# Kernel tuning notes

Hardware: AMD Instinct MI355X
Metric: run time of the kernel (lower is better)

## Reference

```python
import jax, jax.numpy as jnp
import numpy as np

HEAD_SIZE = 16  # matches init_kwargs head_size


def _rope_angles(seq_len, half_dim, base=10000.0):
    # standard RoPE frequencies, matches typical precompute_pos_cis
    freqs = 1.0 / (base ** (np.arange(0, half_dim, dtype=np.float32) / half_dim))
    t = np.arange(seq_len, dtype=np.float32)
    ang = np.outer(t, freqs)  # (S, half_dim)
    return jnp.asarray(np.cos(ang)), jnp.asarray(np.sin(ang))


def setup_inputs() -> dict:
    key = jax.random.key(0)
    ks = jax.random.split(key, 10)
    B, S, D = 2, 2048, 1024
    hd = D // HEAD_SIZE
    pos_cos, pos_sin = _rope_angles(S, hd // 2)
    w = lambda k: jax.random.normal(k, (D, D), jnp.float32) * 0.02
    b = lambda k: jax.random.normal(k, (D,), jnp.float32) * 0.02
    return {
        "x": jax.random.normal(ks[0], (B, S, D), jnp.float32),
        "pos_cos": pos_cos,
        "pos_sin": pos_sin,
        "wq_w": w(ks[1]), "wq_b": b(ks[2]),
        "wk_w": w(ks[3]), "wk_b": b(ks[4]),
        "wv_w": w(ks[5]), "wv_b": b(ks[6]),
        "wo_w": w(ks[7]), "wo_b": b(ks[8]),
    }


def _apply_rope(t, cos, sin):
    # t: (B, S, H, hd); cos/sin: (S, hd//2) -> broadcast (1, S, 1, hd//2)
    B, S, H, hd = t.shape
    tr = t.reshape(B, S, H, hd // 2, 2)
    a, b = tr[..., 0], tr[..., 1]
    c = cos[None, :, None, :]
    s = sin[None, :, None, :]
    # complex multiply (a + ib) * (c + is)
    out_r = a * c - b * s
    out_i = a * s + b * c
    return jnp.stack([out_r, out_i], axis=-1).reshape(B, S, H, hd)


def reference(x, pos_cos, pos_sin, wq_w, wq_b, wk_w, wk_b, wv_w, wv_b, wo_w, wo_b):
    B, S, D = x.shape
    H = HEAD_SIZE
    hd = D // H
    q = (x @ wq_w.T + wq_b).reshape(B, S, H, hd)
    k = (x @ wk_w.T + wk_b).reshape(B, S, H, hd)
    v = (x @ wv_w.T + wv_b).reshape(B, S, H, hd)
    q = _apply_rope(q, pos_cos, pos_sin)
    k = _apply_rope(k, pos_cos, pos_sin)
    scale = 1.0 / jnp.sqrt(jnp.asarray(hd, x.dtype))
    scores = jnp.einsum('bshd,bthd->bhst', q, k) * scale  # (B,H,S,S)
    causal = jnp.tril(jnp.ones((S, S), bool))
    scores = jnp.where(causal[None, None], scores, jnp.asarray(-jnp.inf, scores.dtype))
    probs = jax.nn.softmax(scores, axis=-1)
    out = jnp.einsum('bhst,bthd->bshd', probs, v).reshape(B, S, D)
    return out @ wo_w.T + wo_b
```

## Files before the change

kernel.cpp:

```cpp
#include <hip/hip_runtime.h>
#include <stdint.h>
#include <stddef.h>


typedef __bf16 bf16x8 __attribute__((ext_vector_type(8)));
typedef float  f32x4  __attribute__((ext_vector_type(4)));

__device__ __forceinline__ unsigned short f2b(float f) {
  union { float f; uint32_t u; } v; v.f = f;
  uint32_t u = v.u;
  return (unsigned short)((u + 0x7FFFu + ((u >> 16) & 1u)) >> 16);
}

__device__ __forceinline__ void async16(const void* g, void* l) {
  __builtin_amdgcn_global_load_lds(
      (const __attribute__((address_space(1))) void*)g,
      (__attribute__((address_space(3))) void*)l, 16, 0, 0);
}

__global__ void cast_kernel(const float* __restrict__ in,
                            unsigned short* __restrict__ out, int n4) {
  int i = blockIdx.x * blockDim.x + threadIdx.x;
  if (i >= n4) return;
  float4 v = ((const float4*)in)[i];
  ushort4 o;
  o.x = f2b(v.x); o.y = f2b(v.y); o.z = f2b(v.z); o.w = f2b(v.w);
  ((ushort4*)out)[i] = o;
}

__global__ void cast_w_kernel(const float* __restrict__ wq, const float* __restrict__ wk,
                              const float* __restrict__ wv, const float* __restrict__ wo,
                              unsigned short* __restrict__ wqkv,
                              unsigned short* __restrict__ wobf) {
  int i = blockIdx.x * blockDim.x + threadIdx.x;
  const int sel = i >> 18, k = i & ((1 << 18) - 1);
  const float* src = (sel == 0) ? wq : (sel == 1) ? wk : (sel == 2) ? wv : wo;
  float4 v = ((const float4*)src)[k];
  ushort4 o;
  o.x = f2b(v.x); o.y = f2b(v.y); o.z = f2b(v.z); o.w = f2b(v.w);
  if (sel < 3) ((ushort4*)wqkv)[(size_t)sel * 262144 + k] = o;
  else         ((ushort4*)wobf)[k] = o;
}

__global__ __launch_bounds__(256) void qkv_gemm_kernel(
    const unsigned short* __restrict__ A,
    const unsigned short* __restrict__ W,
    const float* __restrict__ biasq, const float* __restrict__ biask,
    const float* __restrict__ biasv,
    const float* __restrict__ cp, const float* __restrict__ sp,
    unsigned short* __restrict__ qo,
    unsigned short* __restrict__ ko,
    unsigned short* __restrict__ vo)
{
  __shared__ unsigned short As[128 * 64];
  __shared__ unsigned short Bs[128 * 64];
  const int tid  = threadIdx.x;
  const int w    = tid >> 6, l = tid & 63;
  const int lm   = l & 15,  quad = l >> 4;
  const int nblk = blockIdx.x;
  const int m0   = blockIdx.y * 128;
  const int n0g  = nblk * 128;
  const int wm   = (w >> 1) * 64, wn = (w & 1) * 64;

  const f32x4 fzero = {0.f, 0.f, 0.f, 0.f};
  f32x4 acc[4][4];
#pragma unroll
  for (int i = 0; i < 4; ++i)
#pragma unroll
    for (int j = 0; j < 4; ++j) acc[i][j] = fzero;

  for (int k0 = 0; k0 < 1024; k0 += 64) {
    __syncthreads();
#pragma unroll
    for (int q = 0; q < 4; ++q) {
      const int row = w * 16 + lm + (q & 1) * 64;
      const int kc  = quad + (q >> 1) * 4;
      const size_t ldsb = ((size_t)(w + 4 * (q & 1)) * 128 + 64 * (q >> 1)) * 8;
      async16(A + (size_t)(m0 + row) * 1024 + k0 + kc * 8, As + ldsb);
      async16(W + (size_t)(n0g + row) * 1024 + k0 + kc * 8, Bs + ldsb);
    }
    __syncthreads();
#pragma unroll
    for (int kk = 0; kk < 2; ++kk) {
      bf16x8 af[4], bfc[4];
#pragma unroll
      for (int i = 0; i < 4; ++i)
        af[i] = *(const bf16x8*)(As + (size_t)((((w >> 1) * 4 + i) * 128 + kk * 64 + l)) * 8);
#pragma unroll
      for (int j = 0; j < 4; ++j)
        bfc[j] = *(const bf16x8*)(Bs + (size_t)((((w & 1) * 4 + j) * 128 + kk * 64 + l)) * 8);
#pragma unroll
      for (int i = 0; i < 4; ++i)
#pragma unroll
        for (int j = 0; j < 4; ++j)
          acc[i][j] = __builtin_amdgcn_mfma_f32_16x16x32_bf16(af[i], bfc[j], acc[i][j], 0, 0, 0);
    }
  }

  const int which = nblk >> 3;
  const int n0    = (nblk & 7) * 128;
  const float* bias = (which == 0) ? biasq : (which == 1) ? biask : biasv;
#pragma unroll
  for (int i = 0; i < 4; ++i) {
#pragma unroll
    for (int j = 0; j < 4; ++j) {
      const int n = n0 + wn + j * 16 + lm;
      const float bval = bias[n];
      const int h = n >> 6, d = n & 63;
      float vals[4];
#pragma unroll
      for (int r = 0; r < 4; ++r) {
        const int m = m0 + wm + i * 16 + quad * 4 + r;
        const int srow = m & 2047;
        float val = acc[i][j][r] + bval;
        if (which != 2) {
          const float c  = cp[srow * 32 + (d >> 1)];
          const float sn = sp[srow * 32 + (d >> 1)];
          const float part = __shfl_xor(val, 1, 64);
          val = (d & 1) ? (part * sn + val * c) : (val * c - part * sn);
        }
        vals[r] = val;
      }
      const int mbase = m0 + wm + i * 16 + quad * 4;
      const int b = mbase >> 11, s0 = mbase & 2047;
      const int bh = (b << 4) + h;
      if (which == 0) {
#pragma unroll
        for (int r = 0; r < 4; ++r)
          qo[((size_t)bh * 2048 + s0 + r) * 64 + d] = f2b(vals[r]);
      } else if (which == 1) {
#pragma unroll
        for (int r = 0; r < 4; ++r) {
          const int s = s0 + r;
          ko[((size_t)bh * 32 + (s >> 6)) * 4096 +
             (size_t)(((d >> 3) * 64 + (s & 63))) * 8 + (d & 7)] = f2b(vals[r]);
        }
      } else {
        uint32_t w0 = (uint32_t)f2b(vals[0]) | ((uint32_t)f2b(vals[1]) << 16);
        uint32_t w1 = (uint32_t)f2b(vals[2]) | ((uint32_t)f2b(vals[3]) << 16);
        uint2 pk; pk.x = w0; pk.y = w1;
        *(uint2*)(vo + ((size_t)bh * 32 + (s0 >> 6)) * 4096 +
                  (size_t)((((s0 & 63) >> 3) * 64 + d)) * 8 + (s0 & 7)) = pk;
      }
    }
  }
}

__global__ __launch_bounds__(512, 4) void flash_kernel(
    const unsigned short* __restrict__ Q,
    const unsigned short* __restrict__ K,
    const unsigned short* __restrict__ VT,
    unsigned short* __restrict__ O)
{
  constexpr int PSTRIDE = 72;
  __shared__ unsigned short Ks[4096];
  __shared__ unsigned short Vs[4096];
  __shared__ unsigned short Ps[128 * PSTRIDE];
  const int tid = threadIdx.x;
  const int w = tid >> 6, l = tid & 63, lm = l & 15, quad = l >> 4;
  const int bh = blockIdx.x, qb = 15 - blockIdx.y;
  const int mrow_g = qb * 128 + w * 16 + lm;

  const size_t qbase = ((size_t)bh * 2048 + (size_t)qb * 128) * 64;
  bf16x8 aq[2];
#pragma unroll
  for (int kc = 0; kc < 2; ++kc)
    aq[kc] = *(const bf16x8*)(Q + qbase + (size_t)(w * 16 + lm) * 64 + kc * 32 + quad * 8);

  const f32x4 fzero = {0.f, 0.f, 0.f, 0.f};
  f32x4 Oacc[4];
#pragma unroll
  for (int jo = 0; jo < 4; ++jo) Oacc[jo] = fzero;
  float m_i = -1e30f, l_i = 0.f;

  const int nkv = 2 * qb + 2;
  for (int kt = 0; kt < nkv; ++kt) {
    __syncthreads();
    {
      const size_t tbase = ((size_t)bh * 32 + kt) * 4096;
      async16(K  + tbase + (size_t)tid * 8, Ks + (size_t)w * 512);
      async16(VT + tbase + (size_t)tid * 8, Vs + (size_t)w * 512);
    }
    __syncthreads();

    f32x4 Sc[4];
#pragma unroll
    for (int tb = 0; tb < 4; ++tb) Sc[tb] = fzero;
#pragma unroll
    for (int kc = 0; kc < 2; ++kc) {
      bf16x8 ak[4];
#pragma unroll
      for (int tb = 0; tb < 4; ++tb)
        ak[tb] = *(const bf16x8*)(Ks + (size_t)(((kc * 4 + quad) * 64 + tb * 16 + lm)) * 8);
#pragma unroll
      for (int tb = 0; tb < 4; ++tb)
        Sc[tb] = __builtin_amdgcn_mfma_f32_16x16x32_bf16(ak[tb], aq[kc], Sc[tb], 0, 0, 0);
    }

    const bool needmask = (kt * 64 + 63 > qb * 128 + w * 16);
    const int  mrel = mrow_g - kt * 64;
    float mx = -1e30f;
#pragma unroll
    for (int tb = 0; tb < 4; ++tb) {
#pragma unroll
      for (int r = 0; r < 4; ++r) {
        float s = Sc[tb][r] * 0.125f;
        if (needmask && (tb * 16 + quad * 4 + r > mrel)) s = -1e30f;
        Sc[tb][r] = s;
        mx = fmaxf(mx, s);
      }
    }
    mx = fmaxf(mx, __shfl_xor(mx, 16, 64));
    mx = fmaxf(mx, __shfl_xor(mx, 32, 64));
    const float mnew  = fmaxf(m_i, mx);
    const float alpha = __expf(m_i - mnew);
    m_i = mnew;

    float ps = 0.f;
#pragma unroll
    for (int tb = 0; tb < 4; ++tb) {
      float p0 = __expf(Sc[tb][0] - mnew), p1 = __expf(Sc[tb][1] - mnew);
      float p2 = __expf(Sc[tb][2] - mnew), p3 = __expf(Sc[tb][3] - mnew);
      ps += (p0 + p1) + (p2 + p3);
      uint2 pk;
      pk.x = (uint32_t)f2b(p0) | ((uint32_t)f2b(p1) << 16);
      pk.y = (uint32_t)f2b(p2) | ((uint32_t)f2b(p3) << 16);
      *(uint2*)(Ps + (size_t)(w * 16 + lm) * PSTRIDE + tb * 16 + quad * 4) = pk;
    }
    ps += __shfl_xor(ps, 16, 64);
    ps += __shfl_xor(ps, 32, 64);
    l_i = l_i * alpha + ps;

    float af4[4];
#pragma unroll
    for (int r = 0; r < 4; ++r) af4[r] = __shfl(alpha, quad * 4 + r, 64);
#pragma unroll
    for (int jo = 0; jo < 4; ++jo)
#pragma unroll
      for (int r = 0; r < 4; ++r) Oacc[jo][r] *= af4[r];

#pragma unroll
    for (int kc = 0; kc < 2; ++kc) {
      bf16x8 ap = *(const bf16x8*)(Ps + (size_t)(w * 16 + lm) * PSTRIDE + kc * 32 + quad * 8);
      bf16x8 bv[4];
#pragma unroll
      for (int jo = 0; jo < 4; ++jo)
        bv[jo] = *(const bf16x8*)(Vs + (size_t)(((kc * 4 + quad) * 64 + jo * 16 + lm)) * 8);
#pragma unroll
      for (int jo = 0; jo < 4; ++jo)
        Oacc[jo] = __builtin_amdgcn_mfma_f32_16x16x32_bf16(ap, bv[jo], Oacc[jo], 0, 0, 0);
    }
  }

  float lf[4];
#pragma unroll
  for (int r = 0; r < 4; ++r) lf[r] = 1.0f / __shfl(l_i, quad * 4 + r, 64);
  const int b = bh >> 4, h = bh & 15;
#pragma unroll
  for (int jo = 0; jo < 4; ++jo)
#pragma unroll
    for (int r = 0; r < 4; ++r) {
      const int s   = qb * 128 + w * 16 + quad * 4 + r;
      const int col = h * 64 + jo * 16 + lm;
      O[((size_t)b * 2048 + s) * 1024 + col] = f2b(Oacc[jo][r] * lf[r]);
    }
}

__global__ __launch_bounds__(256) void oproj_gemm_kernel(
    const unsigned short* __restrict__ A,
    const unsigned short* __restrict__ W,
    const float* __restrict__ bias,
    float* __restrict__ out)
{
  __shared__ unsigned short As[64 * 64];
  __shared__ unsigned short Bs[128 * 64];
  const int tid = threadIdx.x;
  const int w = tid >> 6, l = tid & 63;
  const int lm = l & 15, quad = l >> 4;
  const int m0 = blockIdx.y * 64;
  const int n0 = blockIdx.x * 128;

  const f32x4 fzero = {0.f, 0.f, 0.f, 0.f};
  f32x4 acc[4][2];
#pragma unroll
  for (int i = 0; i < 4; ++i)
#pragma unroll
    for (int j = 0; j < 2; ++j) acc[i][j] = fzero;

  for (int k0 = 0; k0 < 1024; k0 += 64) {
    __syncthreads();
#pragma unroll
    for (int q = 0; q < 2; ++q) {
      const int row = w * 16 + lm;
      const int kc  = quad + 4 * q;
      async16(A + (size_t)(m0 + row) * 1024 + k0 + kc * 8,
              As + ((size_t)w * 128 + 64 * q) * 8);
    }
#pragma unroll
    for (int q = 0; q < 4; ++q) {
      const int row = w * 16 + lm + (q & 1) * 64;
      const int kc  = quad + 4 * (q >> 1);
      async16(W + (size_t)(n0 + row) * 1024 + k0 + kc * 8,
              Bs + ((size_t)(w + 4 * (q & 1)) * 128 + 64 * (q >> 1)) * 8);
    }
    __syncthreads();
#pragma unroll
    for (int kk = 0; kk < 2; ++kk) {
      bf16x8 af[4], bfc[2];
#pragma unroll
      for (int i = 0; i < 4; ++i)
        af[i] = *(const bf16x8*)(As + (size_t)((i * 128 + kk * 64 + l)) * 8);
#pragma unroll
      for (int j = 0; j < 2; ++j)
        bfc[j] = *(const bf16x8*)(Bs + (size_t)(((w * 2 + j) * 128 + kk * 64 + l)) * 8);
#pragma unroll
      for (int i = 0; i < 4; ++i)
#pragma unroll
        for (int j = 0; j < 2; ++j)
          acc[i][j] = __builtin_amdgcn_mfma_f32_16x16x32_bf16(af[i], bfc[j], acc[i][j], 0, 0, 0);
    }
  }

#pragma unroll
  for (int i = 0; i < 4; ++i) {
#pragma unroll
    for (int j = 0; j < 2; ++j) {
      const int n = n0 + w * 32 + j * 16 + lm;
      const float bval = bias[n];
#pragma unroll
      for (int r = 0; r < 4; ++r) {
        const int m = m0 + i * 16 + quad * 4 + r;
        out[(size_t)m * 1024 + n] = acc[i][j][r] + bval;
      }
    }
  }
}

extern "C" void kernel_launch(void* const* d_in, const int* in_sizes, int n_in,
                              void* d_out, int out_size, void* d_ws, size_t ws_size,
                              hipStream_t stream) {
  (void)in_sizes; (void)n_in; (void)out_size; (void)ws_size;
  const float* x  = (const float*)d_in[0];
  const float* cp = (const float*)d_in[1];
  const float* sp = (const float*)d_in[2];
  const float* wq = (const float*)d_in[3];
  const float* bq = (const float*)d_in[4];
  const float* wk = (const float*)d_in[5];
  const float* bk = (const float*)d_in[6];
  const float* wv = (const float*)d_in[7];
  const float* bv = (const float*)d_in[8];
  const float* wo = (const float*)d_in[9];
  const float* bo = (const float*)d_in[10];
  float* out = (float*)d_out;

  unsigned short* xbf  = (unsigned short*)d_ws;
  unsigned short* wqkv = xbf  + (size_t)4 * 1024 * 1024;
  unsigned short* wobf = wqkv + (size_t)3 * 1024 * 1024;
  unsigned short* qbf  = wobf + (size_t)1 * 1024 * 1024;
  unsigned short* kbf  = qbf  + (size_t)4 * 1024 * 1024;
  unsigned short* vbf  = kbf  + (size_t)4 * 1024 * 1024;
  unsigned short* obf  = vbf  + (size_t)4 * 1024 * 1024;

  hipLaunchKernelGGL(cast_kernel, dim3(4096), dim3(256), 0, stream, x, xbf, 1048576);
  hipLaunchKernelGGL(cast_w_kernel, dim3(4096), dim3(256), 0, stream,
                     wq, wk, wv, wo, wqkv, wobf);

  hipLaunchKernelGGL(qkv_gemm_kernel, dim3(24, 32), dim3(256), 0, stream,
                     xbf, wqkv, bq, bk, bv, cp, sp, qbf, kbf, vbf);
  hipLaunchKernelGGL(flash_kernel, dim3(32, 16), dim3(512), 0, stream,
                     qbf, kbf, vbf, obf);
  hipLaunchKernelGGL(oproj_gemm_kernel, dim3(8, 64), dim3(256), 0, stream,
                     obf, wobf, bo, out);
}
```

Baseline: 240.1 us.

## Double-buffer LDS tiles in QKV GEMM, flash attention, and output projection

Doubles the shared-memory tiles in the QKV GEMM, flash attention, and output-projection kernels. The next K-slice or KV tile is issued asynchronously before computing on the current one, and one barrier per iteration replaces two. This is meant to hide global-to-LDS load latency behind MFMA work. It doubles the LDS footprint per block, which can reduce occupancy, and compiler-inserted waits on async loads may limit the overlap.

```diff
diff --git a/kernel.cpp b/kernel.cpp
--- a/kernel.cpp
+++ b/kernel.cpp
@@ -52,8 +52,8 @@
     unsigned short* __restrict__ ko,
     unsigned short* __restrict__ vo)
 {
-  __shared__ unsigned short As[128 * 64];
-  __shared__ unsigned short Bs[128 * 64];
+  __shared__ unsigned short As[2][128 * 64];
+  __shared__ unsigned short Bs[2][128 * 64];
   const int tid  = threadIdx.x;
   const int w    = tid >> 6, l = tid & 63;
   const int lm   = l & 15,  quad = l >> 4;
@@ -69,33 +69,44 @@
 #pragma unroll
     for (int j = 0; j < 4; ++j) acc[i][j] = fzero;
 
-  for (int k0 = 0; k0 < 1024; k0 += 64) {
-    __syncthreads();
+  auto stage_tile = [&](int buf, int k0) {
 #pragma unroll
     for (int q = 0; q < 4; ++q) {
       const int row = w * 16 + lm + (q & 1) * 64;
       const int kc  = quad + (q >> 1) * 4;
       const size_t ldsb = ((size_t)(w + 4 * (q & 1)) * 128 + 64 * (q >> 1)) * 8;
-      async16(A + (size_t)(m0 + row) * 1024 + k0 + kc * 8, As + ldsb);
-      async16(W + (size_t)(n0g + row) * 1024 + k0 + kc * 8, Bs + ldsb);
-    }
-    __syncthreads();
+      async16(A + (size_t)(m0 + row) * 1024 + k0 + kc * 8, &As[buf][ldsb]);
+      async16(W + (size_t)(n0g + row) * 1024 + k0 + kc * 8, &Bs[buf][ldsb]);
+    }
+  };
+  auto compute_tile = [&](int buf) {
 #pragma unroll
     for (int kk = 0; kk < 2; ++kk) {
       bf16x8 af[4], bfc[4];
 #pragma unroll
       for (int i = 0; i < 4; ++i)
-        af[i] = *(const bf16x8*)(As + (size_t)((((w >> 1) * 4 + i) * 128 + kk * 64 + l)) * 8);
+        af[i] = *(const bf16x8*)(&As[buf][(size_t)((((w >> 1) * 4 + i) * 128 + kk * 64 + l)) * 8]);
 #pragma unroll
       for (int j = 0; j < 4; ++j)
-        bfc[j] = *(const bf16x8*)(Bs + (size_t)((((w & 1) * 4 + j) * 128 + kk * 64 + l)) * 8);
+        bfc[j] = *(const bf16x8*)(&Bs[buf][(size_t)((((w & 1) * 4 + j) * 128 + kk * 64 + l)) * 8]);
 #pragma unroll
       for (int i = 0; i < 4; ++i)
 #pragma unroll
         for (int j = 0; j < 4; ++j)
           acc[i][j] = __builtin_amdgcn_mfma_f32_16x16x32_bf16(af[i], bfc[j], acc[i][j], 0, 0, 0);
     }
+  };
+
+  stage_tile(0, 0);
+  __syncthreads();
+  int cur = 0;
+  for (int t = 0; t < 15; ++t) {
+    stage_tile(cur ^ 1, (t + 1) * 64);
+    compute_tile(cur);
+    __syncthreads();
+    cur ^= 1;
   }
+  compute_tile(cur);
 
   const int which = nblk >> 3;
   const int n0    = (nblk & 7) * 128;
@@ -153,8 +164,8 @@
     unsigned short* __restrict__ O)
 {
   constexpr int PSTRIDE = 72;
-  __shared__ unsigned short Ks[4096];
-  __shared__ unsigned short Vs[4096];
+  __shared__ unsigned short Ks[2][4096];
+  __shared__ unsigned short Vs[2][4096];
   __shared__ unsigned short Ps[128 * PSTRIDE];
   const int tid = threadIdx.x;
   const int w = tid >> 6, l = tid & 63, lm = l & 15, quad = l >> 4;
@@ -173,15 +184,18 @@
   for (int jo = 0; jo < 4; ++jo) Oacc[jo] = fzero;
   float m_i = -1e30f, l_i = 0.f;
 
+  auto stageKV = [&](int buf, int kt) {
+    const size_t tbase = ((size_t)bh * 32 + kt) * 4096;
+    async16(K  + tbase + (size_t)tid * 8, &Ks[buf][(size_t)w * 512]);
+    async16(VT + tbase + (size_t)tid * 8, &Vs[buf][(size_t)w * 512]);
+  };
+
   const int nkv = 2 * qb + 2;
+  stageKV(0, 0);
+  __syncthreads();
+  int cur = 0;
   for (int kt = 0; kt < nkv; ++kt) {
-    __syncthreads();
-    {
-      const size_t tbase = ((size_t)bh * 32 + kt) * 4096;
-      async16(K  + tbase + (size_t)tid * 8, Ks + (size_t)w * 512);
-      async16(VT + tbase + (size_t)tid * 8, Vs + (size_t)w * 512);
-    }
-    __syncthreads();
+    if (kt + 1 < nkv) stageKV(cur ^ 1, kt + 1);
 
     f32x4 Sc[4];
 #pragma unroll
@@ -191,7 +205,7 @@
       bf16x8 ak[4];
 #pragma unroll
       for (int tb = 0; tb < 4; ++tb)
-        ak[tb] = *(const bf16x8*)(Ks + (size_t)(((kc * 4 + quad) * 64 + tb * 16 + lm)) * 8);
+        ak[tb] = *(const bf16x8*)(&Ks[cur][(size_t)(((kc * 4 + quad) * 64 + tb * 16 + lm)) * 8]);
 #pragma unroll
       for (int tb = 0; tb < 4; ++tb)
         Sc[tb] = __builtin_amdgcn_mfma_f32_16x16x32_bf16(ak[tb], aq[kc], Sc[tb], 0, 0, 0);
@@ -245,11 +259,14 @@
       bf16x8 bv[4];
 #pragma unroll
       for (int jo = 0; jo < 4; ++jo)
-        bv[jo] = *(const bf16x8*)(Vs + (size_t)(((kc * 4 + quad) * 64 + jo * 16 + lm)) * 8);
+        bv[jo] = *(const bf16x8*)(&Vs[cur][(size_t)(((kc * 4 + quad) * 64 + jo * 16 + lm)) * 8]);
 #pragma unroll
       for (int jo = 0; jo < 4; ++jo)
         Oacc[jo] = __builtin_amdgcn_mfma_f32_16x16x32_bf16(ap, bv[jo], Oacc[jo], 0, 0, 0);
     }
+
+    __syncthreads();
+    cur ^= 1;
   }
 
   float lf[4];
@@ -272,8 +289,8 @@
     const float* __restrict__ bias,
     float* __restrict__ out)
 {
-  __shared__ unsigned short As[64 * 64];
-  __shared__ unsigned short Bs[128 * 64];
+  __shared__ unsigned short As[2][64 * 64];
+  __shared__ unsigned short Bs[2][128 * 64];
   const int tid = threadIdx.x;
   const int w = tid >> 6, l = tid & 63;
   const int lm = l & 15, quad = l >> 4;
@@ -287,39 +304,50 @@
 #pragma unroll
     for (int j = 0; j < 2; ++j) acc[i][j] = fzero;
 
-  for (int k0 = 0; k0 < 1024; k0 += 64) {
-    __syncthreads();
+  auto stage_tile = [&](int buf, int k0) {
 #pragma unroll
     for (int q = 0; q < 2; ++q) {
       const int row = w * 16 + lm;
       const int kc  = quad + 4 * q;
       async16(A + (size_t)(m0 + row) * 1024 + k0 + kc * 8,
-              As + ((size_t)w * 128 + 64 * q) * 8);
+              &As[buf][((size_t)w * 128 + 64 * q) * 8]);
     }
 #pragma unroll
     for (int q = 0; q < 4; ++q) {
       const int row = w * 16 + lm + (q & 1) * 64;
       const int kc  = quad + 4 * (q >> 1);
       async16(W + (size_t)(n0 + row) * 1024 + k0 + kc * 8,
-              Bs + ((size_t)(w + 4 * (q & 1)) * 128 + 64 * (q >> 1)) * 8);
-    }
-    __syncthreads();
+              &Bs[buf][((size_t)(w + 4 * (q & 1)) * 128 + 64 * (q >> 1)) * 8]);
+    }
+  };
+  auto compute_tile = [&](int buf) {
 #pragma unroll
     for (int kk = 0; kk < 2; ++kk) {
       bf16x8 af[4], bfc[2];
 #pragma unroll
       for (int i = 0; i < 4; ++i)
-        af[i] = *(const bf16x8*)(As + (size_t)((i * 128 + kk * 64 + l)) * 8);
+        af[i] = *(const bf16x8*)(&As[buf][(size_t)((i * 128 + kk * 64 + l)) * 8]);
 #pragma unroll
       for (int j = 0; j < 2; ++j)
-        bfc[j] = *(const bf16x8*)(Bs + (size_t)(((w * 2 + j) * 128 + kk * 64 + l)) * 8);
+        bfc[j] = *(const bf16x8*)(&Bs[buf][(size_t)(((w * 2 + j) * 128 + kk * 64 + l)) * 8]);
 #pragma unroll
       for (int i = 0; i < 4; ++i)
 #pragma unroll
         for (int j = 0; j < 2; ++j)
           acc[i][j] = __builtin_amdgcn_mfma_f32_16x16x32_bf16(af[i], bfc[j], acc[i][j], 0, 0, 0);
     }
+  };
+
+  stage_tile(0, 0);
+  __syncthreads();
+  int cur = 0;
+  for (int t = 0; t < 15; ++t) {
+    stage_tile(cur ^ 1, (t + 1) * 64);
+    compute_tile(cur);
+    __syncthreads();
+    cur ^= 1;
   }
+  compute_tile(cur);
 
 #pragma unroll
   for (int i = 0; i < 4; ++i) {
```

Measured after the change: 281.9 us. 1.17x slower.

## Double-buffer LDS tiles in QKV GEMM, flash attention and output projection

Applied to the files above, without the earlier changes.

Adds a second shared-memory buffer to the QKV GEMM, the flash-attention KV loop and the output-projection GEMM. The async global-to-LDS load of the next tile is issued before computing on the current one, with a single barrier per tile instead of two. The goal is to hide global load latency behind MFMA work. In exchange, LDS use doubles for the staged tiles. For the flash kernel this exceeds what four blocks per CU can share, which may reduce occupancy.

```diff
diff --git a/kernel.cpp b/kernel.cpp
--- a/kernel.cpp
+++ b/kernel.cpp
@@ -52,8 +52,8 @@
     unsigned short* __restrict__ ko,
     unsigned short* __restrict__ vo)
 {
-  __shared__ unsigned short As[128 * 64];
-  __shared__ unsigned short Bs[128 * 64];
+  __shared__ unsigned short As[2][128 * 64];
+  __shared__ unsigned short Bs[2][128 * 64];
   const int tid  = threadIdx.x;
   const int w    = tid >> 6, l = tid & 63;
   const int lm   = l & 15,  quad = l >> 4;
@@ -69,33 +69,49 @@
 #pragma unroll
     for (int j = 0; j < 4; ++j) acc[i][j] = fzero;
 
-  for (int k0 = 0; k0 < 1024; k0 += 64) {
-    __syncthreads();
+  auto stage_tile = [&](unsigned short* Asb, unsigned short* Bsb, int k0) {
 #pragma unroll
     for (int q = 0; q < 4; ++q) {
       const int row = w * 16 + lm + (q & 1) * 64;
       const int kc  = quad + (q >> 1) * 4;
       const size_t ldsb = ((size_t)(w + 4 * (q & 1)) * 128 + 64 * (q >> 1)) * 8;
-      async16(A + (size_t)(m0 + row) * 1024 + k0 + kc * 8, As + ldsb);
-      async16(W + (size_t)(n0g + row) * 1024 + k0 + kc * 8, Bs + ldsb);
-    }
-    __syncthreads();
+      async16(A + (size_t)(m0 + row) * 1024 + k0 + kc * 8, Asb + ldsb);
+      async16(W + (size_t)(n0g + row) * 1024 + k0 + kc * 8, Bsb + ldsb);
+    }
+  };
+  auto compute_tile = [&](const unsigned short* Asb, const unsigned short* Bsb) {
 #pragma unroll
     for (int kk = 0; kk < 2; ++kk) {
       bf16x8 af[4], bfc[4];
 #pragma unroll
       for (int i = 0; i < 4; ++i)
-        af[i] = *(const bf16x8*)(As + (size_t)((((w >> 1) * 4 + i) * 128 + kk * 64 + l)) * 8);
+        af[i] = *(const bf16x8*)(Asb + (size_t)((((w >> 1) * 4 + i) * 128 + kk * 64 + l)) * 8);
 #pragma unroll
       for (int j = 0; j < 4; ++j)
-        bfc[j] = *(const bf16x8*)(Bs + (size_t)((((w & 1) * 4 + j) * 128 + kk * 64 + l)) * 8);
+        bfc[j] = *(const bf16x8*)(Bsb + (size_t)((((w & 1) * 4 + j) * 128 + kk * 64 + l)) * 8);
 #pragma unroll
       for (int i = 0; i < 4; ++i)
 #pragma unroll
         for (int j = 0; j < 4; ++j)
           acc[i][j] = __builtin_amdgcn_mfma_f32_16x16x32_bf16(af[i], bfc[j], acc[i][j], 0, 0, 0);
     }
+  };
+
+  stage_tile(As[0], Bs[0], 0);
+  __syncthreads();
+#pragma unroll 1
+  for (int t = 0; t < 14; t += 2) {
+    stage_tile(As[1], Bs[1], (t + 1) * 64);
+    compute_tile(As[0], Bs[0]);
+    __syncthreads();
+    stage_tile(As[0], Bs[0], (t + 2) * 64);
+    compute_tile(As[1], Bs[1]);
+    __syncthreads();
   }
+  stage_tile(As[1], Bs[1], 15 * 64);
+  compute_tile(As[0], Bs[0]);
+  __syncthreads();
+  compute_tile(As[1], Bs[1]);
 
   const int which = nblk >> 3;
   const int n0    = (nblk & 7) * 128;
@@ -153,8 +169,8 @@
     unsigned short* __restrict__ O)
 {
   constexpr int PSTRIDE = 72;
-  __shared__ unsigned short Ks[4096];
-  __shared__ unsigned short Vs[4096];
+  __shared__ unsigned short Ks[2][4096];
+  __shared__ unsigned short Vs[2][4096];
   __shared__ unsigned short Ps[128 * PSTRIDE];
   const int tid = threadIdx.x;
   const int w = tid >> 6, l = tid & 63, lm = l & 15, quad = l >> 4;
@@ -173,16 +189,13 @@
   for (int jo = 0; jo < 4; ++jo) Oacc[jo] = fzero;
   float m_i = -1e30f, l_i = 0.f;
 
-  const int nkv = 2 * qb + 2;
-  for (int kt = 0; kt < nkv; ++kt) {
-    __syncthreads();
-    {
-      const size_t tbase = ((size_t)bh * 32 + kt) * 4096;
-      async16(K  + tbase + (size_t)tid * 8, Ks + (size_t)w * 512);
-      async16(VT + tbase + (size_t)tid * 8, Vs + (size_t)w * 512);
-    }
-    __syncthreads();
-
+  auto stageKV = [&](unsigned short* Kb, unsigned short* Vb, int kt) {
+    const size_t tbase = ((size_t)bh * 32 + kt) * 4096;
+    async16(K  + tbase + (size_t)tid * 8, Kb + (size_t)w * 512);
+    async16(VT + tbase + (size_t)tid * 8, Vb + (size_t)w * 512);
+  };
+
+  auto kvtile = [&](const unsigned short* Ksb, const unsigned short* Vsb, int kt) {
     f32x4 Sc[4];
 #pragma unroll
     for (int tb = 0; tb < 4; ++tb) Sc[tb] = fzero;
@@ -191,7 +204,7 @@
       bf16x8 ak[4];
 #pragma unroll
       for (int tb = 0; tb < 4; ++tb)
-        ak[tb] = *(const bf16x8*)(Ks + (size_t)(((kc * 4 + quad) * 64 + tb * 16 + lm)) * 8);
+        ak[tb] = *(const bf16x8*)(Ksb + (size_t)(((kc * 4 + quad) * 64 + tb * 16 + lm)) * 8);
 #pragma unroll
       for (int tb = 0; tb < 4; ++tb)
         Sc[tb] = __builtin_amdgcn_mfma_f32_16x16x32_bf16(ak[tb], aq[kc], Sc[tb], 0, 0, 0);
@@ -245,11 +258,24 @@
       bf16x8 bv[4];
 #pragma unroll
       for (int jo = 0; jo < 4; ++jo)
-        bv[jo] = *(const bf16x8*)(Vs + (size_t)(((kc * 4 + quad) * 64 + jo * 16 + lm)) * 8);
+        bv[jo] = *(const bf16x8*)(Vsb + (size_t)(((kc * 4 + quad) * 64 + jo * 16 + lm)) * 8);
 #pragma unroll
       for (int jo = 0; jo < 4; ++jo)
         Oacc[jo] = __builtin_amdgcn_mfma_f32_16x16x32_bf16(ap, bv[jo], Oacc[jo], 0, 0, 0);
     }
+  };
+
+  const int nkv = 2 * qb + 2;
+  stageKV(Ks[0], Vs[0], 0);
+  __syncthreads();
+#pragma unroll 1
+  for (int kt = 0; kt < nkv; kt += 2) {
+    stageKV(Ks[1], Vs[1], kt + 1);
+    kvtile(Ks[0], Vs[0], kt);
+    __syncthreads();
+    if (kt + 2 < nkv) stageKV(Ks[0], Vs[0], kt + 2);
+    kvtile(Ks[1], Vs[1], kt + 1);
+    __syncthreads();
   }
 
   float lf[4];
@@ -272,8 +298,8 @@
     const float* __restrict__ bias,
     float* __restrict__ out)
 {
-  __shared__ unsigned short As[64 * 64];
-  __shared__ unsigned short Bs[128 * 64];
+  __shared__ unsigned short As[2][64 * 64];
+  __shared__ unsigned short Bs[2][128 * 64];
   const int tid = threadIdx.x;
   const int w = tid >> 6, l = tid & 63;
   const int lm = l & 15, quad = l >> 4;
@@ -287,39 +313,55 @@
 #pragma unroll
     for (int j = 0; j < 2; ++j) acc[i][j] = fzero;
 
-  for (int k0 = 0; k0 < 1024; k0 += 64) {
-    __syncthreads();
+  auto stage_tile = [&](unsigned short* Asb, unsigned short* Bsb, int k0) {
 #pragma unroll
     for (int q = 0; q < 2; ++q) {
       const int row = w * 16 + lm;
       const int kc  = quad + 4 * q;
       async16(A + (size_t)(m0 + row) * 1024 + k0 + kc * 8,
-              As + ((size_t)w * 128 + 64 * q) * 8);
+              Asb + ((size_t)w * 128 + 64 * q) * 8);
     }
 #pragma unroll
     for (int q = 0; q < 4; ++q) {
       const int row = w * 16 + lm + (q & 1) * 64;
       const int kc  = quad + 4 * (q >> 1);
       async16(W + (size_t)(n0 + row) * 1024 + k0 + kc * 8,
-              Bs + ((size_t)(w + 4 * (q & 1)) * 128 + 64 * (q >> 1)) * 8);
-    }
-    __syncthreads();
+              Bsb + ((size_t)(w + 4 * (q & 1)) * 128 + 64 * (q >> 1)) * 8);
+    }
+  };
+  auto compute_tile = [&](const unsigned short* Asb, const unsigned short* Bsb) {
 #pragma unroll
     for (int kk = 0; kk < 2; ++kk) {
       bf16x8 af[4], bfc[2];
 #pragma unroll
       for (int i = 0; i < 4; ++i)
-        af[i] = *(const bf16x8*)(As + (size_t)((i * 128 + kk * 64 + l)) * 8);
+        af[i] = *(const bf16x8*)(Asb + (size_t)((i * 128 + kk * 64 + l)) * 8);
 #pragma unroll
       for (int j = 0; j < 2; ++j)
-        bfc[j] = *(const bf16x8*)(Bs + (size_t)(((w * 2 + j) * 128 + kk * 64 + l)) * 8);
+        bfc[j] = *(const bf16x8*)(Bsb + (size_t)(((w * 2 + j) * 128 + kk * 64 + l)) * 8);
 #pragma unroll
       for (int i = 0; i < 4; ++i)
 #pragma unroll
         for (int j = 0; j < 2; ++j)
           acc[i][j] = __builtin_amdgcn_mfma_f32_16x16x32_bf16(af[i], bfc[j], acc[i][j], 0, 0, 0);
     }
+  };
+
+  stage_tile(As[0], Bs[0], 0);
+  __syncthreads();
+#pragma unroll 1
+  for (int t = 0; t < 14; t += 2) {
+    stage_tile(As[1], Bs[1], (t + 1) * 64);
+    compute_tile(As[0], Bs[0]);
+    __syncthreads();
+    stage_tile(As[0], Bs[0], (t + 2) * 64);
+    compute_tile(As[1], Bs[1]);
+    __syncthreads();
   }
+  stage_tile(As[1], Bs[1], 15 * 64);
+  compute_tile(As[0], Bs[0]);
+  __syncthreads();
+  compute_tile(As[1], Bs[1]);
 
 #pragma unroll
   for (int i = 0; i < 4; ++i) {
```

After: 266.0 us. +10.8%, slower.

## Replace async LDS loads with register-staged prefetch pipelining in GEMMs and flash

Applied to the files above, without the earlier changes.

Replaces the direct global-to-LDS async loads in the QKV GEMM, flash attention and output projection kernels with a register-staged software pipeline. The next K-tile (or KV tile) is loaded into registers while the current one is computed from LDS, then written to LDS after a barrier. This aims to hide global memory latency behind MFMA work instead of stalling on the load-and-sync before each tile. In exchange it uses more VGPRs for staging, which may lower occupancy, and it keeps two barriers per iteration.

```diff
diff --git a/kernel.cpp b/kernel.cpp
--- a/kernel.cpp
+++ b/kernel.cpp
@@ -10,12 +10,6 @@
   union { float f; uint32_t u; } v; v.f = f;
   uint32_t u = v.u;
   return (unsigned short)((u + 0x7FFFu + ((u >> 16) & 1u)) >> 16);
-}
-
-__device__ __forceinline__ void async16(const void* g, void* l) {
-  __builtin_amdgcn_global_load_lds(
-      (const __attribute__((address_space(1))) void*)g,
-      (__attribute__((address_space(3))) void*)l, 16, 0, 0);
 }
 
 __global__ void cast_kernel(const float* __restrict__ in,
@@ -52,8 +46,8 @@
     unsigned short* __restrict__ ko,
     unsigned short* __restrict__ vo)
 {
-  __shared__ unsigned short As[128 * 64];
-  __shared__ unsigned short Bs[128 * 64];
+  __shared__ __align__(16) unsigned short As[128 * 64];
+  __shared__ __align__(16) unsigned short Bs[128 * 64];
   const int tid  = threadIdx.x;
   const int w    = tid >> 6, l = tid & 63;
   const int lm   = l & 15,  quad = l >> 4;
@@ -69,17 +63,25 @@
 #pragma unroll
     for (int j = 0; j < 4; ++j) acc[i][j] = fzero;
 
-  for (int k0 = 0; k0 < 1024; k0 += 64) {
-    __syncthreads();
+  uint4 ra[4], rb[4];
+  auto load_regs = [&](int k0) {
 #pragma unroll
     for (int q = 0; q < 4; ++q) {
       const int row = w * 16 + lm + (q & 1) * 64;
       const int kc  = quad + (q >> 1) * 4;
-      const size_t ldsb = ((size_t)(w + 4 * (q & 1)) * 128 + 64 * (q >> 1)) * 8;
-      async16(A + (size_t)(m0 + row) * 1024 + k0 + kc * 8, As + ldsb);
-      async16(W + (size_t)(n0g + row) * 1024 + k0 + kc * 8, Bs + ldsb);
-    }
-    __syncthreads();
+      ra[q] = *(const uint4*)(A + (size_t)(m0 + row) * 1024 + k0 + kc * 8);
+      rb[q] = *(const uint4*)(W + (size_t)(n0g + row) * 1024 + k0 + kc * 8);
+    }
+  };
+  auto write_lds = [&]() {
+#pragma unroll
+    for (int q = 0; q < 4; ++q) {
+      const size_t off = (size_t)(w + 4 * (q & 1)) * 1024 + (size_t)(q >> 1) * 512 + (size_t)l * 8;
+      *(uint4*)(As + off) = ra[q];
+      *(uint4*)(Bs + off) = rb[q];
+    }
+  };
+  auto compute_tile = [&]() {
 #pragma unroll
     for (int kk = 0; kk < 2; ++kk) {
       bf16x8 af[4], bfc[4];
@@ -94,6 +96,20 @@
 #pragma unroll
         for (int j = 0; j < 4; ++j)
           acc[i][j] = __builtin_amdgcn_mfma_f32_16x16x32_bf16(af[i], bfc[j], acc[i][j], 0, 0, 0);
+    }
+  };
+
+  load_regs(0);
+  write_lds();
+  __syncthreads();
+  for (int t = 0; t < 16; ++t) {
+    if (t < 15) load_regs((t + 1) * 64);
+    __builtin_amdgcn_sched_barrier(0);
+    compute_tile();
+    __syncthreads();
+    if (t < 15) {
+      write_lds();
+      __syncthreads();
     }
   }
 
@@ -153,9 +169,9 @@
     unsigned short* __restrict__ O)
 {
   constexpr int PSTRIDE = 72;
-  __shared__ unsigned short Ks[4096];
-  __shared__ unsigned short Vs[4096];
-  __shared__ unsigned short Ps[128 * PSTRIDE];
+  __shared__ __align__(16) unsigned short Ks[4096];
+  __shared__ __align__(16) unsigned short Vs[4096];
+  __shared__ __align__(16) unsigned short Ps[128 * PSTRIDE];
   const int tid = threadIdx.x;
   const int w = tid >> 6, l = tid & 63, lm = l & 15, quad = l >> 4;
   const int bh = blockIdx.x, qb = 15 - blockIdx.y;
@@ -173,16 +189,18 @@
   for (int jo = 0; jo < 4; ++jo) Oacc[jo] = fzero;
   float m_i = -1e30f, l_i = 0.f;
 
-  const int nkv = 2 * qb + 2;
-  for (int kt = 0; kt < nkv; ++kt) {
-    __syncthreads();
-    {
-      const size_t tbase = ((size_t)bh * 32 + kt) * 4096;
-      async16(K  + tbase + (size_t)tid * 8, Ks + (size_t)w * 512);
-      async16(VT + tbase + (size_t)tid * 8, Vs + (size_t)w * 512);
-    }
-    __syncthreads();
-
+  uint4 rk, rv;
+  auto load_regs = [&](int kt) {
+    const size_t tbase = ((size_t)bh * 32 + kt) * 4096;
+    rk = *(const uint4*)(K  + tbase + (size_t)tid * 8);
+    rv = *(const uint4*)(VT + tbase + (size_t)tid * 8);
+  };
+  auto write_lds = [&]() {
+    *(uint4*)(Ks + (size_t)tid * 8) = rk;
+    *(uint4*)(Vs + (size_t)tid * 8) = rv;
+  };
+
+  auto kvtile = [&](int kt) {
     f32x4 Sc[4];
 #pragma unroll
     for (int tb = 0; tb < 4; ++tb) Sc[tb] = fzero;
@@ -250,6 +268,21 @@
       for (int jo = 0; jo < 4; ++jo)
         Oacc[jo] = __builtin_amdgcn_mfma_f32_16x16x32_bf16(ap, bv[jo], Oacc[jo], 0, 0, 0);
     }
+  };
+
+  const int nkv = 2 * qb + 2;
+  load_regs(0);
+  write_lds();
+  __syncthreads();
+  for (int kt = 0; kt < nkv; ++kt) {
+    if (kt + 1 < nkv) load_regs(kt + 1);
+    __builtin_amdgcn_sched_barrier(0);
+    kvtile(kt);
+    __syncthreads();
+    if (kt + 1 < nkv) {
+      write_lds();
+      __syncthreads();
+    }
   }
 
   float lf[4];
@@ -272,8 +305,8 @@
     const float* __restrict__ bias,
     float* __restrict__ out)
 {
-  __shared__ unsigned short As[64 * 64];
-  __shared__ unsigned short Bs[128 * 64];
+  __shared__ __align__(16) unsigned short As[64 * 64];
+  __shared__ __align__(16) unsigned short Bs[128 * 64];
   const int tid = threadIdx.x;
   const int w = tid >> 6, l = tid & 63;
   const int lm = l & 15, quad = l >> 4;
@@ -287,23 +320,30 @@
 #pragma unroll
     for (int j = 0; j < 2; ++j) acc[i][j] = fzero;
 
-  for (int k0 = 0; k0 < 1024; k0 += 64) {
-    __syncthreads();
+  uint4 ra[2], rb[4];
+  auto load_regs = [&](int k0) {
 #pragma unroll
     for (int q = 0; q < 2; ++q) {
       const int row = w * 16 + lm;
       const int kc  = quad + 4 * q;
-      async16(A + (size_t)(m0 + row) * 1024 + k0 + kc * 8,
-              As + ((size_t)w * 128 + 64 * q) * 8);
+      ra[q] = *(const uint4*)(A + (size_t)(m0 + row) * 1024 + k0 + kc * 8);
     }
 #pragma unroll
     for (int q = 0; q < 4; ++q) {
       const int row = w * 16 + lm + (q & 1) * 64;
       const int kc  = quad + 4 * (q >> 1);
-      async16(W + (size_t)(n0 + row) * 1024 + k0 + kc * 8,
-              Bs + ((size_t)(w + 4 * (q & 1)) * 128 + 64 * (q >> 1)) * 8);
-    }
-    __syncthreads();
+      rb[q] = *(const uint4*)(W + (size_t)(n0 + row) * 1024 + k0 + kc * 8);
+    }
+  };
+  auto write_lds = [&]() {
+#pragma unroll
+    for (int q = 0; q < 2; ++q)
+      *(uint4*)(As + (size_t)w * 1024 + (size_t)q * 512 + (size_t)l * 8) = ra[q];
+#pragma unroll
+    for (int q = 0; q < 4; ++q)
+      *(uint4*)(Bs + (size_t)(w + 4 * (q & 1)) * 1024 + (size_t)(q >> 1) * 512 + (size_t)l * 8) = rb[q];
+  };
+  auto compute_tile = [&]() {
 #pragma unroll
     for (int kk = 0; kk < 2; ++kk) {
       bf16x8 af[4], bfc[2];
@@ -318,6 +358,20 @@
 #pragma unroll
         for (int j = 0; j < 2; ++j)
           acc[i][j] = __builtin_amdgcn_mfma_f32_16x16x32_bf16(af[i], bfc[j], acc[i][j], 0, 0, 0);
+    }
+  };
+
+  load_regs(0);
+  write_lds();
+  __syncthreads();
+  for (int t = 0; t < 16; ++t) {
+    if (t < 15) load_regs((t + 1) * 64);
+    __builtin_amdgcn_sched_barrier(0);
+    compute_tile();
+    __syncthreads();
+    if (t < 15) {
+      write_lds();
+      __syncthreads();
     }
   }
 
```

Measured after the change: 389.9 us. 1.62x slower.
